# Optimization experiments

Measured on AMD Instinct MI355X. Metric: run time of the kernel, lower is better.

The kernel has to match this reference:

```python
import jax, jax.numpy as jnp
import numpy as np

# Per-type input feature dims (NODE_DIM values); max dim = 128 = padded width of x.
NODE_DIMS = np.array([16, 32, 64, 128, 64, 32, 16, 128], dtype=np.int32)
N_TYPES = 8
MAX_DIM = 128
FEAT = 256          # node_feature_dim
N_GRAPHS = 100000   # batch_size; one node of each type per graph


def setup_inputs() -> dict:
    key = jax.random.key(0)
    k1, k2, k3 = jax.random.split(key, 3)
    num_nodes = N_GRAPHS * N_TYPES
    x = jax.random.normal(k1, (num_nodes, MAX_DIM), dtype=jnp.float32)
    # Per-type Linear weights, padded to MAX_DIM on the input axis.
    W = jax.random.normal(k2, (N_TYPES, FEAT, MAX_DIM), dtype=jnp.float32) * 0.05
    b = jax.random.normal(k3, (N_TYPES, FEAT), dtype=jnp.float32) * 0.05
    return {"x": x, "W": W, "b": b}


def reference(x, W, b):
    # Node n = g*N_TYPES + k is the type-k node of graph g (the gather index
    # ptr[b] + node_name.index(k) in the original). Dropout is eval-mode (identity).
    # Mask weight columns beyond each type's true input dim: equivalent to
    # slicing x[:, :NODE_DIM[k]] before the per-type Linear.
    mask = (jnp.arange(MAX_DIM)[None, None, :] < jnp.asarray(NODE_DIMS)[:, None, None]).astype(x.dtype)  # [T,1,D]
    W_eff = W * mask  # [T,F,D]
    xg = x.reshape(N_GRAPHS, N_TYPES, MAX_DIM)  # [G,T,D]
    y = jnp.einsum("gtd,tfd->gtf", xg, W_eff) + b[None, :, :]  # [G,T,F]
    return y.reshape(N_GRAPHS * N_TYPES, FEAT)
```

## Files before the change

kernel.cpp:

```cpp
#include <hip/hip_runtime.h>

#define N_GRAPHS 100000
#define NTYPES 8
#define MAXD 128
#define FEAT 256
#define ALDA 136
#define ELDA 68

typedef __attribute__((ext_vector_type(8))) short short8;
typedef __attribute__((ext_vector_type(4))) float f32x4;
typedef __attribute__((ext_vector_type(4))) unsigned uint4v;

constexpr int KSN[NTYPES]  = {1, 1, 2, 4, 2, 1, 1, 4};
constexpr int DIMS[NTYPES] = {16, 32, 64, 128, 64, 32, 16, 128};

__device__ __forceinline__ unsigned f2bf_u(float f) {
    unsigned u = __builtin_bit_cast(unsigned, f);
    return (u + 0x7fffu + ((u >> 16) & 1u)) >> 16;
}
__device__ __forceinline__ unsigned cvt2(float lo, float hi) {
    return f2bf_u(lo) | (f2bf_u(hi) << 16);
}
__device__ __forceinline__ short8 cvt8(f32x4 a, f32x4 b) {
    uint4v u;
    u.x = cvt2(a.x, a.y); u.y = cvt2(a.z, a.w);
    u.z = cvt2(b.x, b.y); u.w = cvt2(b.z, b.w);
    return __builtin_bit_cast(short8, u);
}

__global__ __launch_bounds__(256)
void prepack_w(const float* __restrict__ W, short8* __restrict__ wp)
{
    const int idx  = blockIdx.x * 256 + threadIdx.x;
    const int c16  = idx & 15;
    const int cgrp = (idx >> 4) & 3;
    const int ks   = (idx >> 6) & 3;
    const int ct   = (idx >> 8) & 15;
    const int t    = (idx >> 12) & 7;
    const int col  = ct * 16 + c16;
    const int k    = ks * 32 + cgrp * 8;
    const int dim  = 16 << ((0x30123210u >> (4 * t)) & 0xf);
    const float* src = W + ((size_t)t * FEAT + col) * MAXD + k;
    f32x4 a = *(const f32x4*)src;
    f32x4 b = *(const f32x4*)(src + 4);
    #pragma unroll
    for (int j = 0; j < 4; ++j) {
        if (k + j     >= dim) a[j] = 0.f;
        if (k + 4 + j >= dim) b[j] = 0.f;
    }
    wp[idx] = cvt8(a, b);
}

template<int T, bool PRE>
__device__ __forceinline__ void do_type(const float* __restrict__ x,
                                        const short8* __restrict__ wp,
                                        const float* __restrict__ W,
                                        const float* __restrict__ bias_g,
                                        float* __restrict__ out,
                                        unsigned short* __restrict__ as_,
                                        float* __restrict__ ep,
                                        int g0, int lane, int cgrp, int c16)
{
    constexpr int KS  = KSN[T];
    constexpr int NXT = (T + 1 < NTYPES) ? T + 1 : T;
    constexpr int KSn = KSN[NXT];
    constexpr int SPRn = KSn * 4;

    f32x4 pv[2 * KSn];
    if constexpr (T + 1 < NTYPES) {
        #pragma unroll
        for (int p = 0; p < KSn; ++p) {
            const int idx = p * 64 + lane;
            const int row = idx / SPRn, s8 = idx % SPRn;
            const float* rp = x + (((size_t)(g0 + row)) * NTYPES + (T + 1)) * MAXD + s8 * 8;
            pv[2 * p]     = __builtin_nontemporal_load((const f32x4*)rp);
            pv[2 * p + 1] = __builtin_nontemporal_load((const f32x4*)rp + 1);
        }
    }

    short8 a[KS];
    #pragma unroll
    for (int ks = 0; ks < KS; ++ks)
        a[ks] = *(const short8*)&as_[c16 * ALDA + ks * 32 + cgrp * 8];

    #pragma unroll
    for (int ct4 = 0; ct4 < 4; ++ct4) {
        #pragma unroll
        for (int c = 0; c < 4; ++c) {
            const int ct = ct4 * 4 + c;
            short8 wf[KS];
            if constexpr (PRE) {
                #pragma unroll
                for (int ks = 0; ks < KS; ++ks)
                    wf[ks] = wp[(((T * 16 + ct) * 4 + ks) * 4 + cgrp) * 16 + c16];
            } else {
                constexpr int DIM = DIMS[T];
                #pragma unroll
                for (int ks = 0; ks < KS; ++ks) {
                    const int k = ks * 32 + cgrp * 8;
                    const float* wfp = W + ((size_t)T * FEAT + ct * 16 + c16) * MAXD + k;
                    f32x4 wa = *(const f32x4*)wfp;
                    f32x4 wb = *(const f32x4*)(wfp + 4);
                    #pragma unroll
                    for (int j = 0; j < 4; ++j) {
                        if (k + j     >= DIM) wa[j] = 0.f;
                        if (k + 4 + j >= DIM) wb[j] = 0.f;
                    }
                    wf[ks] = cvt8(wa, wb);
                }
            }
            f32x4 acc = {0.f, 0.f, 0.f, 0.f};
            #pragma unroll
            for (int ks = 0; ks < KS; ++ks)
                acc = __builtin_amdgcn_mfma_f32_16x16x32_bf16(a[ks], wf[ks], acc, 0, 0, 0);
            #pragma unroll
            for (int r = 0; r < 4; ++r)
                ep[(cgrp * 4 + r) * ELDA + (ct & 3) * 16 + c16] = acc[r];
        }
        #pragma unroll
        for (int i = 0; i < 4; ++i) {
            const int row   = i * 4 + (lane >> 4);
            const int coldw = (lane & 15) * 4;
            f32x4 v  = *(const f32x4*)&ep[row * ELDA + coldw];
            f32x4 b4 = *(const f32x4*)&bias_g[T * FEAT + ct4 * 64 + coldw];
            f32x4 res;
            #pragma unroll
            for (int r = 0; r < 4; ++r) res[r] = v[r] + b4[r];
            __builtin_nontemporal_store(res,
                (f32x4*)&out[(((size_t)(g0 + row)) * NTYPES + T) * FEAT + ct4 * 64 + coldw]);
        }
    }

    if constexpr (T + 1 < NTYPES) {
        #pragma unroll
        for (int p = 0; p < KSn; ++p) {
            const int idx = p * 64 + lane;
            const int row = idx / SPRn, s8 = idx % SPRn;
            *(short8*)&as_[row * ALDA + s8 * 8] = cvt8(pv[2 * p], pv[2 * p + 1]);
        }
        do_type<T + 1, PRE>(x, wp, W, bias_g, out, as_, ep, g0, lane, cgrp, c16);
    }
}

template<bool PRE>
__global__ __launch_bounds__(256, 4)
void node_enc(const float* __restrict__ x, const short8* __restrict__ wp,
              const float* __restrict__ W, const float* __restrict__ bias_g,
              float* __restrict__ out)
{
    __shared__ __align__(16) unsigned short As[4][16 * ALDA];
    __shared__ __align__(16) float          Ep[4][16 * ELDA];
    const int tid  = threadIdx.x;
    const int lane = tid & 63;
    const int wave = tid >> 6;
    const int cgrp = lane >> 4;
    const int c16  = lane & 15;
    const int w    = blockIdx.x * 4 + wave;
    if (w >= N_GRAPHS / 16) return;
    const int g0   = w * 16;

    unsigned short* as_ = As[wave];
    {
        const int row = lane >> 2, s8 = lane & 3;
        const float* rp = x + (((size_t)(g0 + row)) * NTYPES + 0) * MAXD + s8 * 8;
        f32x4 v0 = __builtin_nontemporal_load((const f32x4*)rp);
        f32x4 v1 = __builtin_nontemporal_load((const f32x4*)rp + 1);
        *(short8*)&as_[row * ALDA + s8 * 8] = cvt8(v0, v1);
    }

    do_type<0, PRE>(x, wp, W, bias_g, out, as_, Ep[wave], g0, lane, cgrp, c16);
}

extern "C" void kernel_launch(void* const* d_in, const int* in_sizes, int n_in,
                              void* d_out, int out_size, void* d_ws, size_t ws_size,
                              hipStream_t stream)
{
    const float* x = (const float*)d_in[0];
    const float* W = (const float*)d_in[1];
    const float* b = (const float*)d_in[2];
    float* out = (float*)d_out;

    const int grid = (N_GRAPHS / 16 + 3) / 4;
    const size_t wp_bytes = (size_t)32768 * sizeof(short8);

    if (ws_size >= wp_bytes) {
        short8* wp = (short8*)d_ws;
        prepack_w<<<128, 256, 0, stream>>>(W, wp);
        node_enc<true><<<grid, 256, 0, stream>>>(x, wp, W, b, out);
    } else {
        node_enc<false><<<grid, 256, 0, stream>>>(x, nullptr, W, b, out);
    }
}
```

Before: 285.3 us.

## Replace fully unrolled per-type recursion with loops grouped by K-step class

Instead of compile-time recursion that unrolls all eight node types, types are reordered into three classes by K-step count (1, 2, 4), and each class runs a non-unrolled runtime loop. The next type's x tile is still prefetched, now through a runtime switch on its K size. Launch bounds drop from 4 to 3 waves per SIMD. The aim is smaller code and less instruction-cache pressure, at the cost of runtime indexing, branches, and a larger prefetch register array that may lower occupancy.

Result: slower. 299.5 us (+5.0%).

```diff
diff --git a/kernel.cpp b/kernel.cpp
--- a/kernel.cpp
+++ b/kernel.cpp
@@ -6,13 +6,12 @@
 #define FEAT 256
 #define ALDA 136
 #define ELDA 68
+#define ORDER_PACK 0x73426510u
+#define KSN_PACK   0x41124211u
 
 typedef __attribute__((ext_vector_type(8))) short short8;
 typedef __attribute__((ext_vector_type(4))) float f32x4;
 typedef __attribute__((ext_vector_type(4))) unsigned uint4v;
-
-constexpr int KSN[NTYPES]  = {1, 1, 2, 4, 2, 1, 1, 4};
-constexpr int DIMS[NTYPES] = {16, 32, 64, 128, 64, 32, 16, 128};
 
 __device__ __forceinline__ unsigned f2bf_u(float f) {
     unsigned u = __builtin_bit_cast(unsigned, f);
@@ -51,99 +50,121 @@
     wp[idx] = cvt8(a, b);
 }
 
-template<int T, bool PRE>
-__device__ __forceinline__ void do_type(const float* __restrict__ x,
-                                        const short8* __restrict__ wp,
-                                        const float* __restrict__ W,
-                                        const float* __restrict__ bias_g,
-                                        float* __restrict__ out,
-                                        unsigned short* __restrict__ as_,
-                                        float* __restrict__ ep,
-                                        int g0, int lane, int cgrp, int c16)
-{
-    constexpr int KS  = KSN[T];
-    constexpr int NXT = (T + 1 < NTYPES) ? T + 1 : T;
-    constexpr int KSn = KSN[NXT];
-    constexpr int SPRn = KSn * 4;
-
-    f32x4 pv[2 * KSn];
-    if constexpr (T + 1 < NTYPES) {
+template<int KSN_>
+__device__ __forceinline__ void stage_issue(const float* __restrict__ x, int TN,
+                                            int g0, int lane, f32x4* __restrict__ pv)
+{
+    constexpr int SPR = KSN_ * 4;
+    #pragma unroll
+    for (int p = 0; p < KSN_; ++p) {
+        const int idx = p * 64 + lane;
+        const int row = idx / SPR, s8 = idx % SPR;
+        const float* rp = x + (((size_t)(g0 + row)) * NTYPES + TN) * MAXD + s8 * 8;
+        pv[2 * p]     = __builtin_nontemporal_load((const f32x4*)rp);
+        pv[2 * p + 1] = __builtin_nontemporal_load((const f32x4*)rp + 1);
+    }
+}
+template<int KSN_>
+__device__ __forceinline__ void stage_write(unsigned short* __restrict__ as_,
+                                            int lane, const f32x4* __restrict__ pv)
+{
+    constexpr int SPR = KSN_ * 4;
+    #pragma unroll
+    for (int p = 0; p < KSN_; ++p) {
+        const int idx = p * 64 + lane;
+        const int row = idx / SPR, s8 = idx % SPR;
+        *(short8*)&as_[row * ALDA + s8 * 8] = cvt8(pv[2 * p], pv[2 * p + 1]);
+    }
+}
+
+template<int KS, bool PRE>
+__device__ __forceinline__ void do_class(int ib, int ie,
+                                         const float* __restrict__ x,
+                                         const short8* __restrict__ wp,
+                                         const float* __restrict__ W,
+                                         const float* __restrict__ bias_g,
+                                         float* __restrict__ out,
+                                         unsigned short* __restrict__ as_,
+                                         float* __restrict__ ep,
+                                         int g0, int lane, int cgrp, int c16)
+{
+    #pragma unroll 1
+    for (int i = ib; i < ie; ++i) {
+        const int T = (ORDER_PACK >> (4 * i)) & 15;
+
+        short8 a[KS];
         #pragma unroll
-        for (int p = 0; p < KSn; ++p) {
-            const int idx = p * 64 + lane;
-            const int row = idx / SPRn, s8 = idx % SPRn;
-            const float* rp = x + (((size_t)(g0 + row)) * NTYPES + (T + 1)) * MAXD + s8 * 8;
-            pv[2 * p]     = __builtin_nontemporal_load((const f32x4*)rp);
-            pv[2 * p + 1] = __builtin_nontemporal_load((const f32x4*)rp + 1);
+        for (int ks = 0; ks < KS; ++ks)
+            a[ks] = *(const short8*)&as_[c16 * ALDA + ks * 32 + cgrp * 8];
+
+        f32x4 pv[8];
+        int KSn = 0, TN = 0;
+        if (i + 1 < NTYPES) {
+            TN  = (ORDER_PACK >> (4 * (i + 1))) & 15;
+            KSn = (KSN_PACK >> (4 * TN)) & 15;
+            if (KSn == 1)      stage_issue<1>(x, TN, g0, lane, pv);
+            else if (KSn == 2) stage_issue<2>(x, TN, g0, lane, pv);
+            else               stage_issue<4>(x, TN, g0, lane, pv);
         }
-    }
-
-    short8 a[KS];
-    #pragma unroll
-    for (int ks = 0; ks < KS; ++ks)
-        a[ks] = *(const short8*)&as_[c16 * ALDA + ks * 32 + cgrp * 8];
-
-    #pragma unroll
-    for (int ct4 = 0; ct4 < 4; ++ct4) {
+
         #pragma unroll
-        for (int c = 0; c < 4; ++c) {
-            const int ct = ct4 * 4 + c;
-            short8 wf[KS];
-            if constexpr (PRE) {
+        for (int ct4 = 0; ct4 < 4; ++ct4) {
+            #pragma unroll
+            for (int c = 0; c < 4; ++c) {
+                const int ct = ct4 * 4 + c;
+                short8 wf[KS];
+                if constexpr (PRE) {
+                    #pragma unroll
+                    for (int ks = 0; ks < KS; ++ks)
+                        wf[ks] = wp[(((T * 16 + ct) * 4 + ks) * 4 + cgrp) * 16 + c16];
+                } else {
+                    const int dim = 16 << ((0x30123210u >> (4 * T)) & 0xf);
+                    #pragma unroll
+                    for (int ks = 0; ks < KS; ++ks) {
+                        const int k = ks * 32 + cgrp * 8;
+                        const float* wfp = W + ((size_t)T * FEAT + ct * 16 + c16) * MAXD + k;
+                        f32x4 wa = *(const f32x4*)wfp;
+                        f32x4 wb = *(const f32x4*)(wfp + 4);
+                        #pragma unroll
+                        for (int j = 0; j < 4; ++j) {
+                            if (k + j     >= dim) wa[j] = 0.f;
+                            if (k + 4 + j >= dim) wb[j] = 0.f;
+                        }
+                        wf[ks] = cvt8(wa, wb);
+                    }
+                }
+                f32x4 acc = {0.f, 0.f, 0.f, 0.f};
                 #pragma unroll
                 for (int ks = 0; ks < KS; ++ks)
-                    wf[ks] = wp[(((T * 16 + ct) * 4 + ks) * 4 + cgrp) * 16 + c16];
-            } else {
-                constexpr int DIM = DIMS[T];
+                    acc = __builtin_amdgcn_mfma_f32_16x16x32_bf16(a[ks], wf[ks], acc, 0, 0, 0);
                 #pragma unroll
-                for (int ks = 0; ks < KS; ++ks) {
-                    const int k = ks * 32 + cgrp * 8;
-                    const float* wfp = W + ((size_t)T * FEAT + ct * 16 + c16) * MAXD + k;
-                    f32x4 wa = *(const f32x4*)wfp;
-                    f32x4 wb = *(const f32x4*)(wfp + 4);
-                    #pragma unroll
-                    for (int j = 0; j < 4; ++j) {
-                        if (k + j     >= DIM) wa[j] = 0.f;
-                        if (k + 4 + j >= DIM) wb[j] = 0.f;
-                    }
-                    wf[ks] = cvt8(wa, wb);
-                }
+                for (int r = 0; r < 4; ++r)
+                    ep[(cgrp * 4 + r) * ELDA + c * 16 + c16] = acc[r];
             }
-            f32x4 acc = {0.f, 0.f, 0.f, 0.f};
             #pragma unroll
-            for (int ks = 0; ks < KS; ++ks)
-                acc = __builtin_amdgcn_mfma_f32_16x16x32_bf16(a[ks], wf[ks], acc, 0, 0, 0);
-            #pragma unroll
-            for (int r = 0; r < 4; ++r)
-                ep[(cgrp * 4 + r) * ELDA + (ct & 3) * 16 + c16] = acc[r];
+            for (int fi = 0; fi < 4; ++fi) {
+                const int row   = fi * 4 + (lane >> 4);
+                const int coldw = (lane & 15) * 4;
+                f32x4 v  = *(const f32x4*)&ep[row * ELDA + coldw];
+                f32x4 b4 = *(const f32x4*)&bias_g[T * FEAT + ct4 * 64 + coldw];
+                f32x4 res;
+                #pragma unroll
+                for (int r = 0; r < 4; ++r) res[r] = v[r] + b4[r];
+                __builtin_nontemporal_store(res,
+                    (f32x4*)&out[(((size_t)(g0 + row)) * NTYPES + T) * FEAT + ct4 * 64 + coldw]);
+            }
         }
-        #pragma unroll
-        for (int i = 0; i < 4; ++i) {
-            const int row   = i * 4 + (lane >> 4);
-            const int coldw = (lane & 15) * 4;
-            f32x4 v  = *(const f32x4*)&ep[row * ELDA + coldw];
-            f32x4 b4 = *(const f32x4*)&bias_g[T * FEAT + ct4 * 64 + coldw];
-            f32x4 res;
-            #pragma unroll
-            for (int r = 0; r < 4; ++r) res[r] = v[r] + b4[r];
-            __builtin_nontemporal_store(res,
-                (f32x4*)&out[(((size_t)(g0 + row)) * NTYPES + T) * FEAT + ct4 * 64 + coldw]);
+
+        if (i + 1 < NTYPES) {
+            if (KSn == 1)      stage_write<1>(as_, lane, pv);
+            else if (KSn == 2) stage_write<2>(as_, lane, pv);
+            else               stage_write<4>(as_, lane, pv);
         }
     }
-
-    if constexpr (T + 1 < NTYPES) {
-        #pragma unroll
-        for (int p = 0; p < KSn; ++p) {
-            const int idx = p * 64 + lane;
-            const int row = idx / SPRn, s8 = idx % SPRn;
-            *(short8*)&as_[row * ALDA + s8 * 8] = cvt8(pv[2 * p], pv[2 * p + 1]);
-        }
-        do_type<T + 1, PRE>(x, wp, W, bias_g, out, as_, ep, g0, lane, cgrp, c16);
-    }
 }
 
 template<bool PRE>
-__global__ __launch_bounds__(256, 4)
+__global__ __launch_bounds__(256, 3)
 void node_enc(const float* __restrict__ x, const short8* __restrict__ wp,
               const float* __restrict__ W, const float* __restrict__ bias_g,
               float* __restrict__ out)
@@ -160,15 +181,17 @@
     const int g0   = w * 16;
 
     unsigned short* as_ = As[wave];
+    float*          ep  = Ep[wave];
+
     {
-        const int row = lane >> 2, s8 = lane & 3;
-        const float* rp = x + (((size_t)(g0 + row)) * NTYPES + 0) * MAXD + s8 * 8;
-        f32x4 v0 = __builtin_nontemporal_load((const f32x4*)rp);
-        f32x4 v1 = __builtin_nontemporal_load((const f32x4*)rp + 1);
-        *(short8*)&as_[row * ALDA + s8 * 8] = cvt8(v0, v1);
-    }
-
-    do_type<0, PRE>(x, wp, W, bias_g, out, as_, Ep[wave], g0, lane, cgrp, c16);
+        f32x4 pv[2];
+        stage_issue<1>(x, 0, g0, lane, pv);
+        stage_write<1>(as_, lane, pv);
+    }
+
+    do_class<1, PRE>(0, 4, x, wp, W, bias_g, out, as_, ep, g0, lane, cgrp, c16);
+    do_class<2, PRE>(4, 6, x, wp, W, bias_g, out, as_, ep, g0, lane, cgrp, c16);
+    do_class<4, PRE>(6, 8, x, wp, W, bias_g, out, as_, ep, g0, lane, cgrp, c16);
 }
 
 extern "C" void kernel_launch(void* const* d_in, const int* in_sizes, int n_in,
```

## Swap MFMA operands to store output directly, dropping LDS epilogue staging

Applied to the files above, without the earlier changes.

The MFMA operands are swapped (weights as A, node features as B), so each lane's accumulator holds four consecutive output columns of one graph row. Each lane can then add the bias and write a 16-byte vector straight to global memory, which removes the shared-memory epilogue buffer and its write/read round trip. The store also changes from nontemporal to a regular store. The trade-off is that each 16-lane group now writes 64-byte chunks scattered across 16 different rows, instead of the earlier fully contiguous 256-byte row segments, which could reduce write coalescing.

Result: slower. 413.1 us (+44.8%).

```diff
diff --git a/kernel.cpp b/kernel.cpp
--- a/kernel.cpp
+++ b/kernel.cpp
@@ -5,7 +5,6 @@
 #define MAXD 128
 #define FEAT 256
 #define ALDA 136
-#define ELDA 68
 
 typedef __attribute__((ext_vector_type(8))) short short8;
 typedef __attribute__((ext_vector_type(4))) float f32x4;
@@ -58,7 +57,6 @@
                                         const float* __restrict__ bias_g,
                                         float* __restrict__ out,
                                         unsigned short* __restrict__ as_,
-                                        float* __restrict__ ep,
                                         int g0, int lane, int cgrp, int c16)
 {
     constexpr int KS  = KSN[T];
@@ -78,57 +76,44 @@
         }
     }
 
-    short8 a[KS];
+    short8 xf[KS];
     #pragma unroll
     for (int ks = 0; ks < KS; ++ks)
-        a[ks] = *(const short8*)&as_[c16 * ALDA + ks * 32 + cgrp * 8];
+        xf[ks] = *(const short8*)&as_[c16 * ALDA + ks * 32 + cgrp * 8];
 
+    const size_t orow = ((size_t)(g0 + c16) * NTYPES + T) * FEAT;
     #pragma unroll
-    for (int ct4 = 0; ct4 < 4; ++ct4) {
-        #pragma unroll
-        for (int c = 0; c < 4; ++c) {
-            const int ct = ct4 * 4 + c;
-            short8 wf[KS];
-            if constexpr (PRE) {
-                #pragma unroll
-                for (int ks = 0; ks < KS; ++ks)
-                    wf[ks] = wp[(((T * 16 + ct) * 4 + ks) * 4 + cgrp) * 16 + c16];
-            } else {
-                constexpr int DIM = DIMS[T];
-                #pragma unroll
-                for (int ks = 0; ks < KS; ++ks) {
-                    const int k = ks * 32 + cgrp * 8;
-                    const float* wfp = W + ((size_t)T * FEAT + ct * 16 + c16) * MAXD + k;
-                    f32x4 wa = *(const f32x4*)wfp;
-                    f32x4 wb = *(const f32x4*)(wfp + 4);
-                    #pragma unroll
-                    for (int j = 0; j < 4; ++j) {
-                        if (k + j     >= DIM) wa[j] = 0.f;
-                        if (k + 4 + j >= DIM) wb[j] = 0.f;
-                    }
-                    wf[ks] = cvt8(wa, wb);
-                }
-            }
-            f32x4 acc = {0.f, 0.f, 0.f, 0.f};
+    for (int ct = 0; ct < 16; ++ct) {
+        short8 wf[KS];
+        if constexpr (PRE) {
             #pragma unroll
             for (int ks = 0; ks < KS; ++ks)
-                acc = __builtin_amdgcn_mfma_f32_16x16x32_bf16(a[ks], wf[ks], acc, 0, 0, 0);
+                wf[ks] = wp[(((T * 16 + ct) * 4 + ks) * 4 + cgrp) * 16 + c16];
+        } else {
+            constexpr int DIM = DIMS[T];
             #pragma unroll
-            for (int r = 0; r < 4; ++r)
-                ep[(cgrp * 4 + r) * ELDA + (ct & 3) * 16 + c16] = acc[r];
+            for (int ks = 0; ks < KS; ++ks) {
+                const int k = ks * 32 + cgrp * 8;
+                const float* wfp = W + ((size_t)T * FEAT + ct * 16 + c16) * MAXD + k;
+                f32x4 wa = *(const f32x4*)wfp;
+                f32x4 wb = *(const f32x4*)(wfp + 4);
+                #pragma unroll
+                for (int j = 0; j < 4; ++j) {
+                    if (k + j     >= DIM) wa[j] = 0.f;
+                    if (k + 4 + j >= DIM) wb[j] = 0.f;
+                }
+                wf[ks] = cvt8(wa, wb);
+            }
         }
+        f32x4 acc = {0.f, 0.f, 0.f, 0.f};
         #pragma unroll
-        for (int i = 0; i < 4; ++i) {
-            const int row   = i * 4 + (lane >> 4);
-            const int coldw = (lane & 15) * 4;
-            f32x4 v  = *(const f32x4*)&ep[row * ELDA + coldw];
-            f32x4 b4 = *(const f32x4*)&bias_g[T * FEAT + ct4 * 64 + coldw];
-            f32x4 res;
-            #pragma unroll
-            for (int r = 0; r < 4; ++r) res[r] = v[r] + b4[r];
-            __builtin_nontemporal_store(res,
-                (f32x4*)&out[(((size_t)(g0 + row)) * NTYPES + T) * FEAT + ct4 * 64 + coldw]);
-        }
+        for (int ks = 0; ks < KS; ++ks)
+            acc = __builtin_amdgcn_mfma_f32_16x16x32_bf16(wf[ks], xf[ks], acc, 0, 0, 0);
+        const f32x4 b4 = *(const f32x4*)&bias_g[T * FEAT + ct * 16 + cgrp * 4];
+        f32x4 res;
+        #pragma unroll
+        for (int r = 0; r < 4; ++r) res[r] = acc[r] + b4[r];
+        *(f32x4*)&out[orow + ct * 16 + cgrp * 4] = res;
     }
 
     if constexpr (T + 1 < NTYPES) {
@@ -138,7 +123,7 @@
             const int row = idx / SPRn, s8 = idx % SPRn;
             *(short8*)&as_[row * ALDA + s8 * 8] = cvt8(pv[2 * p], pv[2 * p + 1]);
         }
-        do_type<T + 1, PRE>(x, wp, W, bias_g, out, as_, ep, g0, lane, cgrp, c16);
+        do_type<T + 1, PRE>(x, wp, W, bias_g, out, as_, g0, lane, cgrp, c16);
     }
 }
 
@@ -149,7 +134,6 @@
               float* __restrict__ out)
 {
     __shared__ __align__(16) unsigned short As[4][16 * ALDA];
-    __shared__ __align__(16) float          Ep[4][16 * ELDA];
     const int tid  = threadIdx.x;
     const int lane = tid & 63;
     const int wave = tid >> 6;
@@ -168,7 +152,7 @@
         *(short8*)&as_[row * ALDA + s8 * 8] = cvt8(v0, v1);
     }
 
-    do_type<0, PRE>(x, wp, W, bias_g, out, as_, Ep[wave], g0, lane, cgrp, c16);
+    do_type<0, PRE>(x, wp, W, bias_g, out, as_, g0, lane, cgrp, c16);
 }
 
 extern "C" void kernel_launch(void* const* d_in, const int* in_sizes, int n_in,
```
